# Performance work log

Hardware: AMD Instinct MI355X
Metric: run time of the kernel (lower is better)

Reference implementation:

```python
import jax, jax.numpy as jnp
import numpy as np
from jax import lax

D, R, C = 4, 6, 32
P = 2 * R + 1
N = P * P
MR = 12
MP = 2 * MR + 1
MN = MP * MP


def corr_sampler(f_t, f_r, r, dilate):
    # SpatialCorrelationSampler(kernel_size=1, patch_size=2r+1, dilation_patch=dilate)
    # out[b,py,px,y,x] = sum_c f_t[b,c,y,x] * f_r[b,c, y+(py-r)*dilate, x+(px-r)*dilate] (zero pad)
    b, c, h, w = f_t.shape
    p = 2 * r + 1
    pad = r * dilate
    f_r_p = jnp.pad(f_r, ((0, 0), (0, 0), (pad, pad), (pad, pad)))
    offs = jnp.arange(p, dtype=jnp.int32) * dilate
    ii, jj = jnp.meshgrid(offs, offs, indexing='ij')
    shifts = jnp.stack([ii.ravel(), jj.ravel()], 1)  # (p*p, 2)

    def step(_, ij):
        win = lax.dynamic_slice(f_r_p, (0, 0, ij[0], ij[1]), (b, c, h, w))
        return None, jnp.sum(f_t * win, axis=1)  # (b,h,w)

    _, out = lax.scan(step, None, shifts)  # (p*p, b, h, w)
    return out.transpose(1, 0, 2, 3).reshape(b, p, p, h, w)


def bilinear_sample(im, xs, ys):
    # im: (b,c,H,W); xs, ys: (b,h,w) pixel coords; zero padding outside (grid_sample semantics)
    b, c, H, W = im.shape
    x0 = jnp.floor(xs)
    y0 = jnp.floor(ys)
    out = jnp.zeros((b, c) + xs.shape[1:], im.dtype)
    for dy in (0.0, 1.0):
        for dx in (0.0, 1.0):
            xi = x0 + dx
            yi = y0 + dy
            wgt = (1.0 - jnp.abs(xs - xi)) * (1.0 - jnp.abs(ys - yi))
            valid = (xi >= 0) & (xi <= W - 1) & (yi >= 0) & (yi <= H - 1)
            xc = jnp.clip(xi, 0, W - 1).astype(jnp.int32)
            yc = jnp.clip(yi, 0, H - 1).astype(jnp.int32)
            v = jax.vmap(lambda imb, yb, xb: imb[:, yb, xb])(im, yc, xc)  # (b,c,h,w)
            out = out + v * (wgt * valid.astype(im.dtype))[:, None]
    return out


def deform_im2col(im, offset, r):
    # im: (b,c,h,w); offset: (b,h,w,2) with channels (x, y)
    # returns (b, c, (2r+1)^2, h, w), kernel positions row-major over (ky, kx)
    b, c, H, W = im.shape
    h, w = offset.shape[1], offset.shape[2]
    bx = jnp.arange(W, dtype=im.dtype)[None, None, :] + offset[..., 0]  # (b,h,w)
    by = jnp.arange(H, dtype=im.dtype)[None, :, None] + offset[..., 1]
    ks = jnp.arange(-r, r + 1, dtype=im.dtype)
    ky, kx = jnp.meshgrid(ks, ks, indexing='ij')
    koff = jnp.stack([ky.ravel(), kx.ravel()], 1)  # (N, 2) as (ky, kx)

    def step(_, k):
        return None, bilinear_sample(im, bx + k[1], by + k[0])  # (b,c,h,w)

    _, cols = lax.scan(step, None, koff)  # (N,b,c,h,w)
    return cols.transpose(1, 2, 0, 3, 4)


def unfold(x, r):
    # F.unfold(x, kernel_size=2r+1, padding=r) reshaped to (b,c,N,h,w)
    b, c, h, w = x.shape
    p = 2 * r + 1
    xp = jnp.pad(x, ((0, 0), (0, 0), (r, r), (r, r)))
    iy = jnp.arange(p)[:, None] + jnp.arange(h)[None, :]  # (p,h)
    ix = jnp.arange(p)[:, None] + jnp.arange(w)[None, :]  # (p,w)
    win = xp[:, :, iy[:, None, :, None], ix[None, :, None, :]]  # (b,c,p,p,h,w)
    return win.reshape(b, c, p * p, h, w)


def colorizer_forward(feats_r, feats_t, quantized_r, ref_index, current_ind, dil_int):
    ref_list = [int(v) for v in np.asarray(ref_index)]
    nref = feats_r.shape[0]
    gaps = [int(current_ind) - x for x in ref_list]
    nsearch = len([g for g in gaps if g > int(dil_int)])
    dirates = [min(4, g // int(dil_int) + 1) for g in gaps if g > int(dil_int)]
    b, c, h, w = feats_t.shape

    gy, gx = jnp.meshgrid(jnp.arange(-MR, MR + 1, dtype=feats_t.dtype),
                          jnp.arange(-MR, MR + 1, dtype=feats_t.dtype), indexing='ij')
    grid = jnp.stack([gx, gy], -1).reshape(1, MP, MP, 1, 1, 2)

    corrs = []
    offset0 = None
    for i in range(nsearch):
        cc = corr_sampler(feats_t, feats_r[i], MR, dirates[i])  # (b,MP,MP,h,w)
        cc = jax.nn.softmax(cc.reshape(b, MN, h * w), axis=1)
        cc = cc.reshape(b, MP, MP, h, w, 1)
        # expected displacement (x, y); NOTE: original code keeps only the LAST offset0
        offset0 = (cc * grid).sum(axis=(1, 2)) * dirates[i]  # (b,h,w,2)
        col0 = deform_im2col(feats_r[i], offset0, R)  # (b,c,N,h,w)
        corr = (feats_t[:, :, None] * col0).sum(axis=1).reshape(b, N, h * w)
        corrs.append(corr)
    for i in range(nsearch, nref):
        cr = corr_sampler(feats_t, feats_r[i], R, 1).reshape(b, N, h * w)
        corrs.append(cr)

    corr = jax.nn.softmax(jnp.concatenate(corrs, 1), axis=1)[:, None]  # (b,1,nref*N,hw)

    qr = [quantized_r[i][:, :, ::D, ::D] for i in range(nref)]  # prep: stride D (C!=1)
    cols = [deform_im2col(qr[i], offset0, R).reshape(b, C, N, h * w) for i in range(nsearch)]
    cols += [unfold(qr[i], R).reshape(b, C, N, h * w) for i in range(nsearch, nref)]
    image_uf = jnp.concatenate(cols, 2)  # (b,C,nref*N,hw)

    out = (corr * image_uf).sum(axis=2).reshape(b, C, h, w)
    return out


def setup_inputs() -> dict:
    key = jax.random.key(0)
    k1, k2, k3 = jax.random.split(key, 3)
    feats_r = jax.random.normal(k1, (3, 2, 64, 48, 48), jnp.float32) * 0.1
    feats_t = jax.random.normal(k2, (2, 64, 48, 48), jnp.float32) * 0.1
    quantized_r = jax.random.normal(k3, (3, 2, 32, 192, 192), jnp.float32)
    ref_index = np.array([0, 20, 35], dtype=np.int64)
    return {"feats_r": feats_r, "feats_t": feats_t, "quantized_r": quantized_r,
            "ref_index": ref_index, "current_ind": 40, "dil_int": 15}


def reference(feats_r, feats_t, quantized_r, ref_index, current_ind, dil_int):
    return colorizer_forward(feats_r, feats_t, quantized_r, ref_index, current_ind, dil_int)
```

## Files before the change

### kernel.cpp

```cpp
#include <hip/hip_runtime.h>


typedef unsigned short ushort_t;
typedef unsigned int uint_t;
typedef __attribute__((ext_vector_type(8))) short short8;
typedef __attribute__((ext_vector_type(4))) float f32x4;

namespace {
constexpr int NPIX = 2304;
constexpr int FC   = 64;
constexpr int QC   = 32;

constexpr size_t OFS_FTB  = 0;
constexpr size_t OFS_FRB  = OFS_FTB + (size_t)2*NPIX*FC*2;
constexpr size_t OFS_QRCL = OFS_FRB + (size_t)6*NPIX*FC*2;
constexpr size_t OFS_ACC  = OFS_QRCL + (size_t)6*NPIX*QC*4;
constexpr size_t OFS_CORB = OFS_ACC + (size_t)4*NPIX*16*4;
}

__device__ __forceinline__ float blockSum(float v, float* scr) {
  #pragma unroll
  for (int o = 32; o > 0; o >>= 1) v += __shfl_down(v, o);
  const int wid = threadIdx.x >> 6;
  __syncthreads();
  if ((threadIdx.x & 63) == 0) scr[wid] = v;
  __syncthreads();
  float r = scr[0] + scr[1] + scr[2] + scr[3];
  __syncthreads();
  return r;
}

__device__ __forceinline__ ushort_t f2b(float f) {
  uint_t u = __float_as_uint(f);
  return (ushort_t)((u + 0x7fffu + ((u >> 16) & 1u)) >> 16);
}

__global__ __launch_bounds__(256) void pack_all(const float* __restrict__ ft,
                                                const float* __restrict__ fr,
                                                const float* __restrict__ q,
                                                ushort_t* __restrict__ ftb,
                                                ushort_t* __restrict__ frb,
                                                float* __restrict__ qrcl) {
  const int bid = blockIdx.x;
  const int tid = threadIdx.x;
  if (bid < 288) {
    __shared__ float lds[64][65];
    const int mat = bid / 36;
    const int p0  = (bid % 36) * 64;
    const float* src = (mat < 2) ? (ft + (size_t)mat * FC * NPIX)
                                 : (fr + (size_t)(mat - 2) * FC * NPIX);
    ushort_t* dst = (mat < 2) ? (ftb + (size_t)mat * NPIX * FC)
                              : (frb + (size_t)(mat - 2) * NPIX * FC);
    const int lane = tid & 63, row = tid >> 6;
    #pragma unroll
    for (int ch = row; ch < 64; ch += 4)
      lds[ch][lane] = src[(size_t)ch * NPIX + p0 + lane];
    __syncthreads();
    #pragma unroll
    for (int p = row; p < 64; p += 4)
      dst[(size_t)(p0 + p) * FC + lane] = f2b(lds[lane][p]);
  } else {
    __shared__ float lq[32][49];
    const int zz = bid - 288;
    const int ib = zz / 48, yy = zz % 48;
    const float* src = q + (size_t)ib * 32 * 36864 + (size_t)(4 * yy) * 192;
    #pragma unroll
    for (int k = 0; k < 6; ++k) {
      const int l = tid + k * 256;
      const int ch = l / 48, xx = l % 48;
      lq[ch][xx] = src[(size_t)ch * 36864 + 4 * xx];
    }
    __syncthreads();
    float* dst = qrcl + ((size_t)ib * NPIX + yy * 48) * QC;
    #pragma unroll
    for (int k = 0; k < 6; ++k) {
      const int o = tid + k * 256;
      dst[o] = lq[o & 31][o >> 5];
    }
  }
}

template<int MODE>
__device__ __forceinline__ void gram_body(const ushort_t* __restrict__ ftb,
                                          const ushort_t* __restrict__ frb,
                                          float* __restrict__ accb,
                                          float* __restrict__ corb,
                                          int y, int m0, int b, int chunk,
                                          int c0, int c1) {
  constexpr int D_  = (MODE == 0) ? 3 : (MODE == 1) ? 2 : 1;
  constexpr int RAD = (MODE == 2) ? 6 : 12;

  const int lane = threadIdx.x;
  const int col  = lane & 15;
  const int kg   = lane >> 4;

  const short8* ftv = (const short8*)(ftb + ((size_t)b * NPIX + y * 48 + m0 + col) * FC);
  short8 aF0 = ftv[kg];
  short8 aF1 = ftv[4 + kg];

  float wm[3][4], dxv[3][4];
  int sbase[3][4];
  #pragma unroll
  for (int nt = 0; nt < 3; ++nt) {
    #pragma unroll
    for (int r = 0; r < 4; ++r) {
      const int xr   = m0 + kg * 4 + r;
      const int diff = nt * 16 + col - xr;
      const int qd   = diff / D_;
      const bool v   = (diff % D_ == 0) && (qd >= -RAD) && (qd <= RAD);
      wm[nt][r]  = v ? 1.f : 0.f;
      dxv[nt][r] = (float)qd;
      if (MODE == 2) sbase[nt][r] = ((int)b * NPIX + y * 48 + xr) * 169 + (qd + 6);
    }
  }

  const ushort_t* frmat = frb + (size_t)(MODE * 2 + b) * NPIX * FC;
  float se[4] = {0,0,0,0}, sx[4] = {0,0,0,0}, sy[4] = {0,0,0,0};

  for (int dy = c0; dy < c1; ++dy) {
    const int yyr = y + (dy - RAD) * D_;
    if (yyr < 0 || yyr >= 48) continue;
    const float dyv = (float)(dy - RAD);
    const short8* frow = (const short8*)(frmat + (size_t)yyr * 48 * FC);
    #pragma unroll
    for (int nt = 0; nt < 3; ++nt) {
      const short8* bp = frow + (size_t)(nt * 16 + col) * 8;
      short8 b0 = bp[kg], b1 = bp[4 + kg];
      f32x4 c = {0.f, 0.f, 0.f, 0.f};
      c = __builtin_amdgcn_mfma_f32_16x16x32_bf16(aF0, b0, c, 0, 0, 0);
      c = __builtin_amdgcn_mfma_f32_16x16x32_bf16(aF1, b1, c, 0, 0, 0);
      if (MODE < 2) {
        #pragma unroll
        for (int r = 0; r < 4; ++r) {
          const float e = __expf(c[r]) * wm[nt][r];
          se[r] += e;
          sx[r] = fmaf(e, dxv[nt][r], sx[r]);
          sy[r] = fmaf(e, dyv, sy[r]);
        }
      } else {
        #pragma unroll
        for (int r = 0; r < 4; ++r)
          if (wm[nt][r] != 0.f) corb[sbase[nt][r] + dy * 13] = c[r];
      }
    }
  }

  if (MODE < 2) {
    #pragma unroll
    for (int r = 0; r < 4; ++r) {
      #pragma unroll
      for (int m = 1; m <= 8; m <<= 1) {
        se[r] += __shfl_xor(se[r], m);
        sx[r] += __shfl_xor(sx[r], m);
        sy[r] += __shfl_xor(sy[r], m);
      }
    }
    if (col == 0) {
      #pragma unroll
      for (int r = 0; r < 4; ++r) {
        const int p = y * 48 + m0 + kg * 4 + r;
        float* a = accb + ((size_t)(MODE * 2 + b) * NPIX + p) * 16 + chunk * 3;
        a[0] = se[r]; a[1] = sx[r]; a[2] = sy[r];
      }
    }
  }
}

__global__ __launch_bounds__(64) void gram_kernel(const ushort_t* __restrict__ ftb,
                                                  const ushort_t* __restrict__ frb,
                                                  float* __restrict__ accb,
                                                  float* __restrict__ corb) {
  const int y  = blockIdx.x;
  const int m0 = blockIdx.y * 16;
  const int z  = blockIdx.z;
  if (z < 10) {
    const int b = z / 5, chunk = z % 5;
    gram_body<0>(ftb, frb, accb, corb, y, m0, b, chunk, chunk * 5, chunk * 5 + 5);
  } else if (z < 20) {
    const int zz = z - 10;
    const int b = zz / 5, chunk = zz % 5;
    gram_body<1>(ftb, frb, accb, corb, y, m0, b, chunk, chunk * 5, chunk * 5 + 5);
  } else {
    const int zz = z - 20;
    const int b = zz / 3, chunk = zz % 3;
    const int c0 = (chunk == 0) ? 0 : (chunk == 1) ? 5 : 9;
    const int c1 = (chunk == 0) ? 5 : (chunk == 1) ? 9 : 13;
    gram_body<2>(ftb, frb, accb, corb, y, m0, b, chunk, c0, c1);
  }
}

__global__ __launch_bounds__(256) void fuse_kernel(const ushort_t* __restrict__ ftb,
                                                   const ushort_t* __restrict__ frb,
                                                   const float* __restrict__ accb,
                                                   const float* __restrict__ corb,
                                                   const float* __restrict__ qrcl,
                                                   float* __restrict__ out) {
  const int pix = blockIdx.x, b = blockIdx.y;
  const int x = pix % 48, y = pix / 48;
  const int tid = threadIdx.x;
  __shared__ __align__(16) float sD[2][208];
  __shared__ float sp[507];
  __shared__ float soff[4];
  __shared__ float scr[4];
  __shared__ int   gaddr[224];
  __shared__ float gw0[224], gw1[224];
  __shared__ int   gaddr2[192];
  __shared__ float gwq2[192];
  __shared__ __align__(16) float redv[4][8][4];

  if (tid < 2) {
    const int d = (tid == 0) ? 3 : 2;
    const float4* a4 = (const float4*)(accb + ((size_t)(tid * 2 + b) * NPIX + pix) * 16);
    float t[16];
    *(float4*)&t[0]  = a4[0]; *(float4*)&t[4]  = a4[1];
    *(float4*)&t[8]  = a4[2]; *(float4*)&t[12] = a4[3];
    float se = t[0] + t[3] + t[6] + t[9] + t[12];
    float sx = t[1] + t[4] + t[7] + t[10] + t[13];
    float sy = t[2] + t[5] + t[8] + t[11] + t[14];
    const int klox = max(-12, -(x / d)), khix = min(12, (47 - x) / d);
    const int kloy = max(-12, -(y / d)), khiy = min(12, (47 - y) / d);
    const int nvx = khix - klox + 1, nvy = khiy - kloy + 1;
    const int svx = (klox + khix) * nvx / 2, svy = (kloy + khiy) * nvy / 2;
    se += (float)(625 - nvx * nvy);
    sx -= (float)(nvy * svx);
    sy -= (float)(nvx * svy);
    soff[tid * 2 + 0] = (float)d * sx / se;
    soff[tid * 2 + 1] = (float)d * sy / se;
  }
  __syncthreads();

  const float bxf0 = floorf((float)x + soff[0]), byf0 = floorf((float)y + soff[1]);
  const float bxf1 = floorf((float)x + soff[2]), byf1 = floorf((float)y + soff[3]);
  const float fx0 = (float)x + soff[0] - bxf0, fy0 = (float)y + soff[1] - byf0;
  const float fx1 = (float)x + soff[2] - bxf1, fy1 = (float)y + soff[3] - byf1;
  const int bx00 = (int)bxf0 - 6, by00 = (int)byf0 - 6;
  const int bx01 = (int)bxf1 - 6, by01 = (int)byf1 - 6;

  {
    const int lane = tid & 63, wv = tid >> 6;
    const int arow = lane & 15, kg = lane >> 4;
    const short8* ftv = (const short8*)(ftb + ((size_t)b * NPIX + pix) * FC);
    const short8 bF0 = ftv[kg], bF1 = ftv[4 + kg];
    for (int gi = wv; gi < 26; gi += 4) {
      const bool r1 = (gi >= 13);
      const int grp = r1 ? gi - 13 : gi;
      const int g = grp * 16 + arow;
      short8 a0 = {0,0,0,0,0,0,0,0}, a1 = {0,0,0,0,0,0,0,0};
      if (g < 196) {
        const int gy = (r1 ? by01 : by00) + g / 14;
        const int gx = (r1 ? bx01 : bx00) + g % 14;
        if (gy >= 0 && gy < 48 && gx >= 0 && gx < 48) {
          const short8* fp = (const short8*)(frb + ((size_t)((r1 ? 2 : 0) + b) * NPIX + gy * 48 + gx) * FC);
          a0 = fp[kg]; a1 = fp[4 + kg];
        }
      }
      f32x4 c = {0.f, 0.f, 0.f, 0.f};
      c = __builtin_amdgcn_mfma_f32_16x16x32_bf16(a0, bF0, c, 0, 0, 0);
      c = __builtin_amdgcn_mfma_f32_16x16x32_bf16(a1, bF1, c, 0, 0, 0);
      if (arow == 0)
        *(f32x4*)&sD[r1 ? 1 : 0][grp * 16 + kg * 4] = c;
    }
  }
  __syncthreads();

  float ls = 0.f;
  for (int s = tid; s < 507; s += 256) {
    float v;
    if (s < 338) {
      const bool r1 = (s >= 169);
      const int n = r1 ? s - 169 : s;
      const float fx = r1 ? fx1 : fx0, fy = r1 ? fy1 : fy0;
      const float w00 = (1.f - fy) * (1.f - fx), w01 = (1.f - fy) * fx;
      const float w10 = fy * (1.f - fx),        w11 = fy * fx;
      const int a_ = n / 13, c2 = n % 13;
      const float* Dp = r1 ? sD[1] : sD[0];
      v = w00 * Dp[a_ * 14 + c2]       + w01 * Dp[a_ * 14 + c2 + 1]
        + w10 * Dp[(a_ + 1) * 14 + c2] + w11 * Dp[(a_ + 1) * 14 + c2 + 1];
    } else {
      const int n = s - 338;
      const int yy = y + n / 13 - 6, xx = x + n % 13 - 6;
      v = (yy >= 0 && yy < 48 && xx >= 0 && xx < 48)
            ? corb[((size_t)b * NPIX + pix) * 169 + n] : 0.f;
    }
    const float e = __expf(v);
    sp[s] = e; ls += e;
  }
  ls = blockSum(ls, scr);
  const float inv = 1.f / ls;

  if (tid < 224) {
    if (tid < 196) {
      const int ty = tid / 14, tx = tid % 14;
      const float w00 = (1.f - fy1) * (1.f - fx1), w01 = (1.f - fy1) * fx1;
      const float w10 = fy1 * (1.f - fx1),        w11 = fy1 * fx1;
      auto P = [&](const float* base, int a, int c2) -> float {
        return (a >= 0 && a < 13 && c2 >= 0 && c2 < 13) ? base[a * 13 + c2] : 0.f;
      };
      const float s0 = w00 * P(sp, ty, tx)     + w01 * P(sp, ty, tx - 1)
                     + w10 * P(sp, ty - 1, tx) + w11 * P(sp, ty - 1, tx - 1);
      const float s1 = w00 * P(sp + 169, ty, tx)     + w01 * P(sp + 169, ty, tx - 1)
                     + w10 * P(sp + 169, ty - 1, tx) + w11 * P(sp + 169, ty - 1, tx - 1);
      const int gy = by01 + ty, gx = bx01 + tx;
      const bool v = (gy >= 0 && gy < 48 && gx >= 0 && gx < 48);
      gaddr[tid] = v ? (gy * 48 + gx) * QC : 0;
      gw0[tid] = v ? s0 : 0.f;
      gw1[tid] = v ? s1 : 0.f;
    } else {
      gaddr[tid] = 0; gw0[tid] = 0.f; gw1[tid] = 0.f;
    }
  }
  if (tid < 192) {
    if (tid < 169) {
      const int yy = y + tid / 13 - 6, xx = x + tid % 13 - 6;
      const bool v = (yy >= 0 && yy < 48 && xx >= 0 && xx < 48);
      gaddr2[tid] = v ? (yy * 48 + xx) * QC : 0;
      gwq2[tid] = v ? sp[338 + tid] : 0.f;
    } else {
      gaddr2[tid] = 0; gwq2[tid] = 0.f;
    }
  }
  __syncthreads();

  const int lane = tid & 63, wv = tid >> 6;
  const int chgrp = lane & 7, ssub = lane >> 3;
  const float* q0 = qrcl + (size_t)(0 + b) * NPIX * QC + chgrp * 4;
  const float* q1 = qrcl + (size_t)(2 + b) * NPIX * QC + chgrp * 4;
  const float* q2 = qrcl + (size_t)(4 + b) * NPIX * QC + chgrp * 4;
  float4 acc = {0.f, 0.f, 0.f, 0.f};
  #pragma unroll
  for (int it = 0; it < 7; ++it) {
    const int s = it * 32 + wv * 8 + ssub;
    const int a = gaddr[s];
    const float w0 = gw0[s], w1 = gw1[s];
    const float4 v0 = *(const float4*)(q0 + a);
    const float4 v1 = *(const float4*)(q1 + a);
    acc.x = fmaf(w0, v0.x, acc.x); acc.y = fmaf(w0, v0.y, acc.y);
    acc.z = fmaf(w0, v0.z, acc.z); acc.w = fmaf(w0, v0.w, acc.w);
    acc.x = fmaf(w1, v1.x, acc.x); acc.y = fmaf(w1, v1.y, acc.y);
    acc.z = fmaf(w1, v1.z, acc.z); acc.w = fmaf(w1, v1.w, acc.w);
  }
  #pragma unroll
  for (int it = 0; it < 6; ++it) {
    const int s = it * 32 + wv * 8 + ssub;
    const int a = gaddr2[s];
    const float w = gwq2[s];
    const float4 v2 = *(const float4*)(q2 + a);
    acc.x = fmaf(w, v2.x, acc.x); acc.y = fmaf(w, v2.y, acc.y);
    acc.z = fmaf(w, v2.z, acc.z); acc.w = fmaf(w, v2.w, acc.w);
  }
  #pragma unroll
  for (int off = 8; off <= 32; off <<= 1) {
    acc.x += __shfl_xor(acc.x, off);
    acc.y += __shfl_xor(acc.y, off);
    acc.z += __shfl_xor(acc.z, off);
    acc.w += __shfl_xor(acc.w, off);
  }
  if (ssub == 0) *(float4*)redv[wv][chgrp] = acc;
  __syncthreads();
  if (tid < 8) {
    float4 r0 = *(float4*)redv[0][tid], r1 = *(float4*)redv[1][tid];
    float4 r2 = *(float4*)redv[2][tid], r3 = *(float4*)redv[3][tid];
    const float o0 = (r0.x + r1.x + r2.x + r3.x) * inv;
    const float o1 = (r0.y + r1.y + r2.y + r3.y) * inv;
    const float o2 = (r0.z + r1.z + r2.z + r3.z) * inv;
    const float o3 = (r0.w + r1.w + r2.w + r3.w) * inv;
    float* op = out + ((size_t)(b * 32 + tid * 4) * 48 + y) * 48 + x;
    op[0] = o0; op[NPIX] = o1; op[2 * NPIX] = o2; op[3 * NPIX] = o3;
  }
}

extern "C" void kernel_launch(void* const* d_in, const int* in_sizes, int n_in,
                              void* d_out, int out_size, void* d_ws, size_t ws_size,
                              hipStream_t stream) {
  (void)in_sizes; (void)n_in; (void)out_size; (void)ws_size;
  const float* feats_r     = (const float*)d_in[0];
  const float* feats_t     = (const float*)d_in[1];
  const float* quantized_r = (const float*)d_in[2];
  char* ws = (char*)d_ws;
  ushort_t* ftb  = (ushort_t*)(ws + OFS_FTB);
  ushort_t* frb  = (ushort_t*)(ws + OFS_FRB);
  float*    qrcl = (float*)(ws + OFS_QRCL);
  float*    accb = (float*)(ws + OFS_ACC);
  float*    corb = (float*)(ws + OFS_CORB);

  pack_all<<<576, 256, 0, stream>>>(feats_t, feats_r, quantized_r, ftb, frb, qrcl);
  gram_kernel<<<dim3(48, 3, 26), 64, 0, stream>>>(ftb, frb, accb, corb);
  fuse_kernel<<<dim3(NPIX, 2), 256, 0, stream>>>(ftb, frb, accb, corb, qrcl, (float*)d_out);
}
```

Measured before the change: 140.3 us.

## Map one wavefront per pixel in fuse kernel, replacing block reductions with shuffles

The fuse kernel now processes two pixels per 128-thread block, with one 64-lane wavefront owning each pixel end to end. The softmax sum and the final output reduction become wave shuffles, which removes the cross-wave LDS reductions and several barriers. The corb loads are hoisted to the start so they overlap the MFMA stage, and LDS buffers are reused for the second gather table. Each wave now does four times the serial work per pixel (all 26 MFMA groups and the full gather loop), trading per-pixel latency for less synchronisation and more concurrent blocks.

```diff
diff --git a/kernel.cpp b/kernel.cpp
--- a/kernel.cpp
+++ b/kernel.cpp
@@ -16,18 +16,6 @@
 constexpr size_t OFS_QRCL = OFS_FRB + (size_t)6*NPIX*FC*2;
 constexpr size_t OFS_ACC  = OFS_QRCL + (size_t)6*NPIX*QC*4;
 constexpr size_t OFS_CORB = OFS_ACC + (size_t)4*NPIX*16*4;
-}
-
-__device__ __forceinline__ float blockSum(float v, float* scr) {
-  #pragma unroll
-  for (int o = 32; o > 0; o >>= 1) v += __shfl_down(v, o);
-  const int wid = threadIdx.x >> 6;
-  __syncthreads();
-  if ((threadIdx.x & 63) == 0) scr[wid] = v;
-  __syncthreads();
-  float r = scr[0] + scr[1] + scr[2] + scr[3];
-  __syncthreads();
-  return r;
 }
 
 __device__ __forceinline__ ushort_t f2b(float f) {
@@ -189,28 +177,51 @@
   }
 }
 
-__global__ __launch_bounds__(256) void fuse_kernel(const ushort_t* __restrict__ ftb,
-                                                   const ushort_t* __restrict__ frb,
-                                                   const float* __restrict__ accb,
-                                                   const float* __restrict__ corb,
-                                                   const float* __restrict__ qrcl,
-                                                   float* __restrict__ out) {
-  const int pix = blockIdx.x, b = blockIdx.y;
+__global__ __launch_bounds__(128, 6) void fuse_kernel(const ushort_t* __restrict__ ftb,
+                                                      const ushort_t* __restrict__ frb,
+                                                      const float* __restrict__ accb,
+                                                      const float* __restrict__ corb,
+                                                      const float* __restrict__ qrcl,
+                                                      float* __restrict__ out) {
+  const int tid = threadIdx.x;
+  const int wv = tid >> 6, lane = tid & 63;
+  const int b = blockIdx.y;
+  const int pix = blockIdx.x * 2 + wv;
   const int x = pix % 48, y = pix / 48;
-  const int tid = threadIdx.x;
-  __shared__ __align__(16) float sD[2][208];
-  __shared__ float sp[507];
-  __shared__ float soff[4];
-  __shared__ float scr[4];
-  __shared__ int   gaddr[224];
-  __shared__ float gw0[224], gw1[224];
-  __shared__ int   gaddr2[192];
-  __shared__ float gwq2[192];
-  __shared__ __align__(16) float redv[4][8][4];
-
-  if (tid < 2) {
-    const int d = (tid == 0) ? 3 : 2;
-    const float4* a4 = (const float4*)(accb + ((size_t)(tid * 2 + b) * NPIX + pix) * 16);
+
+  __shared__ __align__(16) float sDu[2][416];
+  __shared__ float sp[2][512];
+  __shared__ int   gaddr[2][224];
+  __shared__ float gw0[2][224], gw1[2][224];
+
+  const int kgB = lane >> 4;
+  const short8* ftv = (const short8*)(ftb + ((size_t)b * NPIX + pix) * FC);
+  const short8 bF0 = ftv[kgB], bF1 = ftv[4 + kgB];
+
+  float cv5 = 0.f, cv6 = 0.f, cv7 = 0.f;
+  {
+    const float* cb = corb + ((size_t)b * NPIX + pix) * 169;
+    int n = lane - 18;
+    if (n >= 0) {
+      const int yy = y + n / 13 - 6, xx = x + n % 13 - 6;
+      if (yy >= 0 && yy < 48 && xx >= 0 && xx < 48) cv5 = cb[n];
+    }
+    n = lane + 46;
+    {
+      const int yy = y + n / 13 - 6, xx = x + n % 13 - 6;
+      if (yy >= 0 && yy < 48 && xx >= 0 && xx < 48) cv6 = cb[n];
+    }
+    n = lane + 110;
+    if (n < 169) {
+      const int yy = y + n / 13 - 6, xx = x + n % 13 - 6;
+      if (yy >= 0 && yy < 48 && xx >= 0 && xx < 48) cv7 = cb[n];
+    }
+  }
+
+  float vox = 0.f, voy = 0.f;
+  if (lane < 2) {
+    const int d = (lane == 0) ? 3 : 2;
+    const float4* a4 = (const float4*)(accb + ((size_t)(lane * 2 + b) * NPIX + pix) * 16);
     float t[16];
     *(float4*)&t[0]  = a4[0]; *(float4*)&t[4]  = a4[1];
     *(float4*)&t[8]  = a4[2]; *(float4*)&t[12] = a4[3];
@@ -224,28 +235,29 @@
     se += (float)(625 - nvx * nvy);
     sx -= (float)(nvy * svx);
     sy -= (float)(nvx * svy);
-    soff[tid * 2 + 0] = (float)d * sx / se;
-    soff[tid * 2 + 1] = (float)d * sy / se;
-  }
-  __syncthreads();
-
-  const float bxf0 = floorf((float)x + soff[0]), byf0 = floorf((float)y + soff[1]);
-  const float bxf1 = floorf((float)x + soff[2]), byf1 = floorf((float)y + soff[3]);
-  const float fx0 = (float)x + soff[0] - bxf0, fy0 = (float)y + soff[1] - byf0;
-  const float fx1 = (float)x + soff[2] - bxf1, fy1 = (float)y + soff[3] - byf1;
+    vox = (float)d * sx / se;
+    voy = (float)d * sy / se;
+  }
+  const float ox0 = __shfl(vox, 0), oy0 = __shfl(voy, 0);
+  const float ox1 = __shfl(vox, 1), oy1 = __shfl(voy, 1);
+
+  const float bxf0 = floorf((float)x + ox0), byf0 = floorf((float)y + oy0);
+  const float bxf1 = floorf((float)x + ox1), byf1 = floorf((float)y + oy1);
+  const float fx0 = (float)x + ox0 - bxf0, fy0 = (float)y + oy0 - byf0;
+  const float fx1 = (float)x + ox1 - bxf1, fy1 = (float)y + oy1 - byf1;
   const int bx00 = (int)bxf0 - 6, by00 = (int)byf0 - 6;
   const int bx01 = (int)bxf1 - 6, by01 = (int)byf1 - 6;
 
   {
-    const int lane = tid & 63, wv = tid >> 6;
     const int arow = lane & 15, kg = lane >> 4;
-    const short8* ftv = (const short8*)(ftb + ((size_t)b * NPIX + pix) * FC);
-    const short8 bF0 = ftv[kg], bF1 = ftv[4 + kg];
-    for (int gi = wv; gi < 26; gi += 4) {
-      const bool r1 = (gi >= 13);
+    const short8 z8 = {0,0,0,0,0,0,0,0};
+    float* sDw = sDu[wv];
+    #pragma unroll 2
+    for (int gi = 0; gi < 26; ++gi) {
+      const bool r1 = gi >= 13;
       const int grp = r1 ? gi - 13 : gi;
       const int g = grp * 16 + arow;
-      short8 a0 = {0,0,0,0,0,0,0,0}, a1 = {0,0,0,0,0,0,0,0};
+      short8 a0 = z8, a1 = z8;
       if (g < 196) {
         const int gy = (r1 ? by01 : by00) + g / 14;
         const int gx = (r1 ? bx01 : bx00) + g % 14;
@@ -258,80 +270,101 @@
       c = __builtin_amdgcn_mfma_f32_16x16x32_bf16(a0, bF0, c, 0, 0, 0);
       c = __builtin_amdgcn_mfma_f32_16x16x32_bf16(a1, bF1, c, 0, 0, 0);
       if (arow == 0)
-        *(f32x4*)&sD[r1 ? 1 : 0][grp * 16 + kg * 4] = c;
+        *(f32x4*)&sDw[(r1 ? 208 : 0) + grp * 16 + kg * 4] = c;
     }
   }
   __syncthreads();
 
   float ls = 0.f;
-  for (int s = tid; s < 507; s += 256) {
-    float v;
-    if (s < 338) {
-      const bool r1 = (s >= 169);
-      const int n = r1 ? s - 169 : s;
-      const float fx = r1 ? fx1 : fx0, fy = r1 ? fy1 : fy0;
-      const float w00 = (1.f - fy) * (1.f - fx), w01 = (1.f - fy) * fx;
-      const float w10 = fy * (1.f - fx),        w11 = fy * fx;
-      const int a_ = n / 13, c2 = n % 13;
-      const float* Dp = r1 ? sD[1] : sD[0];
-      v = w00 * Dp[a_ * 14 + c2]       + w01 * Dp[a_ * 14 + c2 + 1]
-        + w10 * Dp[(a_ + 1) * 14 + c2] + w11 * Dp[(a_ + 1) * 14 + c2 + 1];
-    } else {
-      const int n = s - 338;
-      const int yy = y + n / 13 - 6, xx = x + n % 13 - 6;
-      v = (yy >= 0 && yy < 48 && xx >= 0 && xx < 48)
-            ? corb[((size_t)b * NPIX + pix) * 169 + n] : 0.f;
-    }
-    const float e = __expf(v);
-    sp[s] = e; ls += e;
-  }
-  ls = blockSum(ls, scr);
+  {
+    float* spw = sp[wv];
+    const float* sD0 = sDu[wv];
+    const float* sD1 = sDu[wv] + 208;
+    #pragma unroll
+    for (int k = 0; k < 8; ++k) {
+      const int s = lane + 64 * k;
+      if (s < 507) {
+        float v;
+        if (s < 338) {
+          const bool r1 = (s >= 169);
+          const unsigned n = r1 ? s - 169 : s;
+          const float fx = r1 ? fx1 : fx0, fy = r1 ? fy1 : fy0;
+          const float w00 = (1.f - fy) * (1.f - fx), w01 = (1.f - fy) * fx;
+          const float w10 = fy * (1.f - fx),        w11 = fy * fx;
+          const unsigned a_ = n / 13u, c2 = n % 13u;
+          const float* Dp = r1 ? sD1 : sD0;
+          v = w00 * Dp[a_ * 14 + c2]       + w01 * Dp[a_ * 14 + c2 + 1]
+            + w10 * Dp[(a_ + 1) * 14 + c2] + w11 * Dp[(a_ + 1) * 14 + c2 + 1];
+        } else {
+          v = (k == 5) ? cv5 : (k == 6) ? cv6 : cv7;
+        }
+        const float e = __expf(v);
+        spw[s] = e; ls += e;
+      }
+    }
+  }
+  #pragma unroll
+  for (int o = 1; o <= 32; o <<= 1) ls += __shfl_xor(ls, o);
   const float inv = 1.f / ls;
-
-  if (tid < 224) {
-    if (tid < 196) {
-      const int ty = tid / 14, tx = tid % 14;
-      const float w00 = (1.f - fy1) * (1.f - fx1), w01 = (1.f - fy1) * fx1;
-      const float w10 = fy1 * (1.f - fx1),        w11 = fy1 * fx1;
-      auto P = [&](const float* base, int a, int c2) -> float {
-        return (a >= 0 && a < 13 && c2 >= 0 && c2 < 13) ? base[a * 13 + c2] : 0.f;
-      };
-      const float s0 = w00 * P(sp, ty, tx)     + w01 * P(sp, ty, tx - 1)
-                     + w10 * P(sp, ty - 1, tx) + w11 * P(sp, ty - 1, tx - 1);
-      const float s1 = w00 * P(sp + 169, ty, tx)     + w01 * P(sp + 169, ty, tx - 1)
-                     + w10 * P(sp + 169, ty - 1, tx) + w11 * P(sp + 169, ty - 1, tx - 1);
-      const int gy = by01 + ty, gx = bx01 + tx;
-      const bool v = (gy >= 0 && gy < 48 && gx >= 0 && gx < 48);
-      gaddr[tid] = v ? (gy * 48 + gx) * QC : 0;
-      gw0[tid] = v ? s0 : 0.f;
-      gw1[tid] = v ? s1 : 0.f;
-    } else {
-      gaddr[tid] = 0; gw0[tid] = 0.f; gw1[tid] = 0.f;
-    }
-  }
-  if (tid < 192) {
-    if (tid < 169) {
-      const int yy = y + tid / 13 - 6, xx = x + tid % 13 - 6;
-      const bool v = (yy >= 0 && yy < 48 && xx >= 0 && xx < 48);
-      gaddr2[tid] = v ? (yy * 48 + xx) * QC : 0;
-      gwq2[tid] = v ? sp[338 + tid] : 0.f;
-    } else {
-      gaddr2[tid] = 0; gwq2[tid] = 0.f;
-    }
-  }
   __syncthreads();
 
-  const int lane = tid & 63, wv = tid >> 6;
+  int*   gaddr2 = (int*)sDu[wv];
+  float* gwq2   = sDu[wv] + 208;
+  {
+    const float* spw = sp[wv];
+    const float w00 = (1.f - fy1) * (1.f - fx1), w01 = (1.f - fy1) * fx1;
+    const float w10 = fy1 * (1.f - fx1),        w11 = fy1 * fx1;
+    #pragma unroll
+    for (int j = 0; j < 4; ++j) {
+      const int t = lane + 64 * j;
+      if (t < 224) {
+        if (t < 196) {
+          const int ty = t / 14, tx = t % 14;
+          auto P = [&](const float* base, int a, int c2) -> float {
+            return (a >= 0 && a < 13 && c2 >= 0 && c2 < 13) ? base[a * 13 + c2] : 0.f;
+          };
+          const float s0 = w00 * P(spw, ty, tx)     + w01 * P(spw, ty, tx - 1)
+                         + w10 * P(spw, ty - 1, tx) + w11 * P(spw, ty - 1, tx - 1);
+          const float s1 = w00 * P(spw + 169, ty, tx)     + w01 * P(spw + 169, ty, tx - 1)
+                         + w10 * P(spw + 169, ty - 1, tx) + w11 * P(spw + 169, ty - 1, tx - 1);
+          const int gy = by01 + ty, gx = bx01 + tx;
+          const bool v = (gy >= 0 && gy < 48 && gx >= 0 && gx < 48);
+          gaddr[wv][t] = v ? (gy * 48 + gx) * QC : 0;
+          gw0[wv][t] = v ? s0 : 0.f;
+          gw1[wv][t] = v ? s1 : 0.f;
+        } else {
+          gaddr[wv][t] = 0; gw0[wv][t] = 0.f; gw1[wv][t] = 0.f;
+        }
+      }
+    }
+    #pragma unroll
+    for (int j = 0; j < 3; ++j) {
+      const int t = lane + 64 * j;
+      if (t < 169) {
+        const int yy = y + t / 13 - 6, xx = x + t % 13 - 6;
+        const bool v = (yy >= 0 && yy < 48 && xx >= 0 && xx < 48);
+        gaddr2[t] = v ? (yy * 48 + xx) * QC : 0;
+        gwq2[t] = v ? spw[338 + t] : 0.f;
+      } else {
+        gaddr2[t] = 0; gwq2[t] = 0.f;
+      }
+    }
+  }
+  __syncthreads();
+
   const int chgrp = lane & 7, ssub = lane >> 3;
   const float* q0 = qrcl + (size_t)(0 + b) * NPIX * QC + chgrp * 4;
   const float* q1 = qrcl + (size_t)(2 + b) * NPIX * QC + chgrp * 4;
   const float* q2 = qrcl + (size_t)(4 + b) * NPIX * QC + chgrp * 4;
   float4 acc = {0.f, 0.f, 0.f, 0.f};
-  #pragma unroll
-  for (int it = 0; it < 7; ++it) {
-    const int s = it * 32 + wv * 8 + ssub;
-    const int a = gaddr[s];
-    const float w0 = gw0[s], w1 = gw1[s];
+  const int* ga = gaddr[wv];
+  const float* w0p = gw0[wv];
+  const float* w1p = gw1[wv];
+  #pragma unroll 4
+  for (int it = 0; it < 28; ++it) {
+    const int s = it * 8 + ssub;
+    const int a = ga[s];
+    const float w0 = w0p[s], w1 = w1p[s];
     const float4 v0 = *(const float4*)(q0 + a);
     const float4 v1 = *(const float4*)(q1 + a);
     acc.x = fmaf(w0, v0.x, acc.x); acc.y = fmaf(w0, v0.y, acc.y);
@@ -339,9 +372,9 @@
     acc.x = fmaf(w1, v1.x, acc.x); acc.y = fmaf(w1, v1.y, acc.y);
     acc.z = fmaf(w1, v1.z, acc.z); acc.w = fmaf(w1, v1.w, acc.w);
   }
-  #pragma unroll
-  for (int it = 0; it < 6; ++it) {
-    const int s = it * 32 + wv * 8 + ssub;
+  #pragma unroll 4
+  for (int it = 0; it < 24; ++it) {
+    const int s = it * 8 + ssub;
     const int a = gaddr2[s];
     const float w = gwq2[s];
     const float4 v2 = *(const float4*)(q2 + a);
@@ -355,17 +388,12 @@
     acc.z += __shfl_xor(acc.z, off);
     acc.w += __shfl_xor(acc.w, off);
   }
-  if (ssub == 0) *(float4*)redv[wv][chgrp] = acc;
-  __syncthreads();
-  if (tid < 8) {
-    float4 r0 = *(float4*)redv[0][tid], r1 = *(float4*)redv[1][tid];
-    float4 r2 = *(float4*)redv[2][tid], r3 = *(float4*)redv[3][tid];
-    const float o0 = (r0.x + r1.x + r2.x + r3.x) * inv;
-    const float o1 = (r0.y + r1.y + r2.y + r3.y) * inv;
-    const float o2 = (r0.z + r1.z + r2.z + r3.z) * inv;
-    const float o3 = (r0.w + r1.w + r2.w + r3.w) * inv;
-    float* op = out + ((size_t)(b * 32 + tid * 4) * 48 + y) * 48 + x;
-    op[0] = o0; op[NPIX] = o1; op[2 * NPIX] = o2; op[3 * NPIX] = o3;
+  if (ssub == 0) {
+    float* op = out + ((size_t)(b * 32 + chgrp * 4) * 48 + y) * 48 + x;
+    op[0]        = acc.x * inv;
+    op[NPIX]     = acc.y * inv;
+    op[2 * NPIX] = acc.z * inv;
+    op[3 * NPIX] = acc.w * inv;
   }
 }
 
@@ -385,5 +413,5 @@
 
   pack_all<<<576, 256, 0, stream>>>(feats_t, feats_r, quantized_r, ftb, frb, qrcl);
   gram_kernel<<<dim3(48, 3, 26), 64, 0, stream>>>(ftb, frb, accb, corb);
-  fuse_kernel<<<dim3(NPIX, 2), 256, 0, stream>>>(ftb, frb, accb, corb, qrcl, (float*)d_out);
-}
+  fuse_kernel<<<dim3(NPIX / 2, 2), 128, 0, stream>>>(ftb, frb, accb, corb, qrcl, (float*)d_out);
+}
```

Result: no change. 140.7 us (+0.2%).
